# Kernel optimization log

Hardware: AMD Instinct MI355X
Metric: run time of the kernel (lower is better)

The kernel has to match this reference:

```python
import jax, jax.numpy as jnp
import numpy as np


def setup_inputs() -> dict:
    key = jax.random.key(0)
    k1, k2, k3 = jax.random.split(key, 3)
    B, S, H, D, W = 2, 2048, 16, 128, 4  # W = world_size (ring steps); k,v carry W*S total KV
    q = jax.random.normal(k1, (B, S, H, D), dtype=jnp.float32)
    k = jax.random.normal(k2, (B, W * S, H, D), dtype=jnp.float32)
    v = jax.random.normal(k3, (B, W * S, H, D), dtype=jnp.float32)
    return {"q": q, "k": k, "v": v}


def _ring_attention(q, k, v):
    # q: [B,S,H,D]; k,v: [B,W*S,H,D] -- W ring steps over KV chunks of length S
    B, S, H, D = q.shape
    W = k.shape[1] // S
    scale = D ** -0.5
    kc = k.reshape(B, W, S, H, D).transpose(1, 0, 2, 3, 4)  # [W,B,S,H,D]
    vc = v.reshape(B, W, S, H, D).transpose(1, 0, 2, 3, 4)
    o0 = jnp.zeros((B, H, S, D), q.dtype)
    l0 = jnp.zeros((B, H, S, 1), q.dtype)
    m0 = jnp.full((B, H, S, 1), -jnp.inf, q.dtype)

    def step(carry, kv):
        o, l, m = carry
        kb, vb = kv  # [B,S,H,D]
        scores = jnp.einsum('bqhd,bkhd->bhqk', q, kb) * scale  # [B,H,S,S]
        m_blk = jnp.max(scores, axis=-1, keepdims=True)
        p = jnp.exp(scores - m_blk)
        l_blk = jnp.sum(p, axis=-1, keepdims=True)
        m_new = jnp.maximum(m, m_blk)
        alpha = jnp.exp(m - m_blk * 0 - m_new) if False else jnp.exp(m - m_new)
        beta = jnp.exp(m_blk - m_new)
        l_new = alpha * l + beta * l_blk
        o_blk = jnp.einsum('bhqk,bkhd->bhqd', p, vb)
        o_new = (alpha * o * l + beta * o_blk) / l_new  # online-softmax rescale (same as torch code)
        return (o_new, l_new, m_new), None

    (o, l, m), _ = jax.lax.scan(step, (o0, l0, m0), (kc, vc))
    return o.transpose(0, 2, 1, 3)  # back to [B,S,H,D]


def reference(q, k, v):
    return _ring_attention(q, k, v)
```

## Files before the change

### kernel.cpp

```cpp
#include <hip/hip_runtime.h>

namespace {
constexpr int Bc  = 2;
constexpr int Sq  = 2048;
constexpr int Hn  = 16;
constexpr int Dd  = 128;
constexpr int Skv = 8192;
constexpr int TK  = 64;
constexpr int NT  = Skv / TK;
constexpr int QT  = 256;
constexpr int PP  = 72;
constexpr int PV  = 132;
constexpr int TILE_ELEMS = TK * Dd;
constexpr int QTF = 128;
constexpr int KPF = 136;
constexpr float C_EXP = (float)(0.08838834764831845 * 1.4426950408889634);
}

typedef __attribute__((ext_vector_type(8))) short short8;
typedef __attribute__((ext_vector_type(8))) unsigned short us8;
typedef __attribute__((ext_vector_type(4))) float f32x4;
typedef __attribute__((ext_vector_type(4))) unsigned short us4;

__device__ __forceinline__ unsigned short f2bf(float f) {
  unsigned int u = __builtin_bit_cast(unsigned int, f);
  u += 0x7fffu + ((u >> 16) & 1u);
  return (unsigned short)(u >> 16);
}

__device__ __forceinline__ void gload16(const unsigned short* g, unsigned short* l) {
  __builtin_amdgcn_global_load_lds(
      (__attribute__((address_space(1))) void*)(g),
      (__attribute__((address_space(3))) void*)(l), 16, 0, 0);
}

__global__ __launch_bounds__(256) void convert_kernel(
    const float* __restrict__ kg, const float* __restrict__ vg,
    unsigned short* __restrict__ kws, unsigned short* __restrict__ vws) {
  __shared__ unsigned short lds_v[TK * PV];

  const int t = threadIdx.x;
  const int bid = blockIdx.x;
  const int bh = bid >> 7;
  const int tile = bid & 127;
  const int b = bh >> 4, h = bh & (Hn - 1);
  const size_t HD = (size_t)Hn * Dd;

  const float* kin = kg + ((size_t)b * Skv + (size_t)tile * TK) * HD + (size_t)h * Dd;
  const float* vin = vg + ((size_t)b * Skv + (size_t)tile * TK) * HD + (size_t)h * Dd;
  unsigned short* kout = kws + (size_t)bid * TILE_ELEMS;
  unsigned short* vout = vws + (size_t)bid * TILE_ELEMS;

  {
    const int key = t >> 2;
    const int c   = t & 3;
    const float* vrow = vin + (size_t)key * HD + c * 32;
    unsigned short* lrow = &lds_v[key * PV + c * 32];
#pragma unroll
    for (int j = 0; j < 8; ++j) {
      float4 a = *(const float4*)(vrow + 4 * j);
      us4 w;
      w[0] = f2bf(a.x); w[1] = f2bf(a.y); w[2] = f2bf(a.z); w[3] = f2bf(a.w);
      *(us4*)&lrow[4 * j] = w;
    }
  }

  {
    const int key = t >> 2;
    const float* krow = kin + (size_t)key * HD;
    unsigned short* orow = kout + key * Dd;
#pragma unroll
    for (int i = 0; i < 4; ++i) {
      const int dblk = (t & 3) * 4 + i;
      const int dsrc = dblk ^ (key & 7);
      float4 a = *(const float4*)(krow + dsrc * 8);
      float4 c4 = *(const float4*)(krow + dsrc * 8 + 4);
      us8 w;
      w[0] = f2bf(a.x);  w[1] = f2bf(a.y);  w[2] = f2bf(a.z);  w[3] = f2bf(a.w);
      w[4] = f2bf(c4.x); w[5] = f2bf(c4.y); w[6] = f2bf(c4.z); w[7] = f2bf(c4.w);
      *(us8*)&orow[dblk * 8] = w;
    }
  }

  __syncthreads();

  {
    const int d = t >> 1;
    const int half = t & 1;
    const int f = (d >> 1) & 7;
#pragma unroll
    for (int jj = 0; jj < 4; ++jj) {
      const int kp = half * 4 + jj;
      const int sb = kp ^ f;
      us8 w;
#pragma unroll
      for (int r = 0; r < 8; ++r) w[r] = lds_v[(sb * 8 + r) * PV + d];
      *(us8*)&vout[d * TK + kp * 8] = w;
    }
  }
}

__global__ __launch_bounds__(512, 2) void ring_attn_bf16(
    const float* __restrict__ qg, const unsigned short* __restrict__ kws,
    const unsigned short* __restrict__ vws, float* __restrict__ og) {
  __shared__ unsigned short lds_k[2][TK * Dd];
  __shared__ unsigned short lds_vt[2][Dd * TK];
  __shared__ unsigned short lds_p[8 * 32 * PP];

  const int t    = threadIdx.x;
  const int wave = t >> 6;
  const int lane = t & 63;
  const int l15  = lane & 15;
  const int quad = lane >> 4;
  const int bid  = blockIdx.x;
  const int bh = ((bid & 7) << 2) | (bid >> 6);
  const int qt = (bid >> 3) & 7;
  const int h  = bh & (Hn - 1);
  const int b  = bh >> 4;
  const size_t HD = (size_t)Hn * Dd;

  const unsigned short* kbh = kws + (size_t)bh * (NT * (size_t)TILE_ELEMS);
  const unsigned short* vbh = vws + (size_t)bh * (NT * (size_t)TILE_ELEMS);
  const int c0 = wave * 1024 + lane * 8;

#pragma unroll
  for (int j = 0; j < 2; ++j) {
    gload16(kbh + c0 + j * 512, &lds_k[0][wave * 1024 + j * 512]);
    gload16(vbh + c0 + j * 512, &lds_vt[0][wave * 1024 + j * 512]);
  }

  short8 qfrag[2][4];
  {
    const float* qbase = qg + ((size_t)b * Sq) * HD + (size_t)h * Dd;
#pragma unroll
    for (int mt = 0; mt < 2; ++mt) {
      const int qrow = qt * QT + wave * 32 + mt * 16 + l15;
      const float* qp = qbase + (size_t)qrow * HD;
#pragma unroll
      for (int kk = 0; kk < 4; ++kk) {
        const float* p8 = qp + kk * 32 + quad * 8;
        float4 a = *(const float4*)p8;
        float4 c = *(const float4*)(p8 + 4);
        short8 f;
        f[0] = (short)f2bf(a.x); f[1] = (short)f2bf(a.y);
        f[2] = (short)f2bf(a.z); f[3] = (short)f2bf(a.w);
        f[4] = (short)f2bf(c.x); f[5] = (short)f2bf(c.y);
        f[6] = (short)f2bf(c.z); f[7] = (short)f2bf(c.w);
        qfrag[mt][kk] = f;
      }
    }
  }

  f32x4 acco[2][8];
#pragma unroll
  for (int mt = 0; mt < 2; ++mt)
#pragma unroll
    for (int n = 0; n < 8; ++n)
      acco[mt][n] = (f32x4){0.f, 0.f, 0.f, 0.f};

  float l_part[2] = {0.f, 0.f};

  int koff[4], voff[2];
#pragma unroll
  for (int kk = 0; kk < 4; ++kk) koff[kk] = ((kk * 4 + quad) ^ (l15 & 7)) * 8;
#pragma unroll
  for (int kk = 0; kk < 2; ++kk) voff[kk] = ((kk * 4 + quad) ^ ((l15 >> 1) & 7)) * 8;

  asm volatile("s_waitcnt vmcnt(0)" ::: "memory");
  __syncthreads();

  int buf = 0;
  for (int it = 0; it < NT; ++it) {
    if (it + 1 < NT) {
      const unsigned short* kt = kbh + (size_t)(it + 1) * TILE_ELEMS;
      const unsigned short* vt = vbh + (size_t)(it + 1) * TILE_ELEMS;
      unsigned short* kd = &lds_k[buf ^ 1][wave * 1024];
      unsigned short* vd = &lds_vt[buf ^ 1][wave * 1024];
#pragma unroll
      for (int j = 0; j < 2; ++j) {
        gload16(kt + c0 + j * 512, kd + j * 512);
        gload16(vt + c0 + j * 512, vd + j * 512);
      }
    }

    const unsigned short* kb = &lds_k[buf][0];
    f32x4 accs[2][4];
#pragma unroll
    for (int mt = 0; mt < 2; ++mt)
#pragma unroll
      for (int n = 0; n < 4; ++n)
        accs[mt][n] = (f32x4){0.f, 0.f, 0.f, 0.f};

    __builtin_amdgcn_s_setprio(1);
#pragma unroll
    for (int n = 0; n < 4; ++n) {
      short8 bfr[4];
#pragma unroll
      for (int kk = 0; kk < 4; ++kk)
        bfr[kk] = *(const short8*)&kb[(n * 16 + l15) * Dd + koff[kk]];
#pragma unroll
      for (int mt = 0; mt < 2; ++mt)
#pragma unroll
        for (int kk = 0; kk < 4; ++kk)
          accs[mt][n] = __builtin_amdgcn_mfma_f32_16x16x32_bf16(
              bfr[kk], qfrag[mt][kk], accs[mt][n], 0, 0, 0);
    }
    __builtin_amdgcn_s_setprio(0);

#pragma unroll
    for (int mt = 0; mt < 2; ++mt) {
      float lacc = 0.f;
#pragma unroll
      for (int n = 0; n < 4; ++n) {
        float s0 = __builtin_amdgcn_exp2f(accs[mt][n][0] * C_EXP);
        float s1 = __builtin_amdgcn_exp2f(accs[mt][n][1] * C_EXP);
        float s2 = __builtin_amdgcn_exp2f(accs[mt][n][2] * C_EXP);
        float s3 = __builtin_amdgcn_exp2f(accs[mt][n][3] * C_EXP);
        lacc += (s0 + s1) + (s2 + s3);
        us4 w;
        w[0] = f2bf(s0); w[1] = f2bf(s1); w[2] = f2bf(s2); w[3] = f2bf(s3);
        *(us4*)&lds_p[wave * (32 * PP) + (mt * 16 + l15) * PP + n * 16 + quad * 4] = w;
      }
      l_part[mt] += lacc;
    }

    asm volatile("s_waitcnt lgkmcnt(0)" ::: "memory");

    const unsigned short* vb = &lds_vt[buf][0];
    __builtin_amdgcn_s_setprio(1);
#pragma unroll
    for (int kk = 0; kk < 2; ++kk) {
      short8 afr[2];
#pragma unroll
      for (int mt = 0; mt < 2; ++mt)
        afr[mt] = *(const short8*)&lds_p[wave * (32 * PP) + (mt * 16 + l15) * PP +
                                         kk * 32 + quad * 8];
#pragma unroll
      for (int n = 0; n < 8; ++n) {
        short8 bfr = *(const short8*)&vb[(n * 16 + l15) * TK + voff[kk]];
        acco[0][n] = __builtin_amdgcn_mfma_f32_16x16x32_bf16(afr[0], bfr, acco[0][n], 0, 0, 0);
        acco[1][n] = __builtin_amdgcn_mfma_f32_16x16x32_bf16(afr[1], bfr, acco[1][n], 0, 0, 0);
      }
    }
    __builtin_amdgcn_s_setprio(0);

    asm volatile("s_waitcnt vmcnt(0)" ::: "memory");
    __syncthreads();
    buf ^= 1;
  }

#pragma unroll
  for (int mt = 0; mt < 2; ++mt) {
    float l = l_part[mt];
    l += __shfl_xor(l, 16);
    l += __shfl_xor(l, 32);
    l_part[mt] = l;
  }

  float* ob = og + ((size_t)b * Sq) * HD + (size_t)h * Dd;
#pragma unroll
  for (int mt = 0; mt < 2; ++mt) {
#pragma unroll
    for (int i = 0; i < 4; ++i) {
      const int qrow = qt * QT + wave * 32 + mt * 16 + quad * 4 + i;
      const float inv = 1.0f / __shfl(l_part[mt], quad * 4 + i);
      float* op = ob + (size_t)qrow * HD;
#pragma unroll
      for (int n = 0; n < 8; ++n)
        op[n * 16 + l15] = acco[mt][n][i] * inv;
    }
  }
}

__global__ __launch_bounds__(256) void ring_attn_fallback(
    const float* __restrict__ qg, const float* __restrict__ kg,
    const float* __restrict__ vg, float* __restrict__ og) {
  __shared__ unsigned short lds_k[TK * KPF];
  __shared__ unsigned short lds_vt[Dd * 64];
  __shared__ unsigned short lds_p[4 * 32 * PP];

  const int t    = threadIdx.x;
  const int wave = t >> 6;
  const int lane = t & 63;
  const int l15  = lane & 15;
  const int quad = lane >> 4;
  const int bid  = blockIdx.x;
  const int bh = ((bid & 7) << 2) | (bid >> 7);
  const int qt = (bid >> 3) & 15;
  const int h  = bh & (Hn - 1);
  const int b  = bh >> 4;
  const size_t HD = (size_t)Hn * Dd;

  short8 qfrag[2][4];
  {
    const float* qbase = qg + ((size_t)b * Sq) * HD + (size_t)h * Dd;
    for (int mt = 0; mt < 2; ++mt) {
      const int qrow = qt * QTF + wave * 32 + mt * 16 + l15;
      const float* qp = qbase + (size_t)qrow * HD;
#pragma unroll
      for (int kk = 0; kk < 4; ++kk) {
        const float* p8 = qp + kk * 32 + quad * 8;
        float4 a = *(const float4*)p8;
        float4 c = *(const float4*)(p8 + 4);
        short8 f;
        f[0] = (short)f2bf(a.x); f[1] = (short)f2bf(a.y);
        f[2] = (short)f2bf(a.z); f[3] = (short)f2bf(a.w);
        f[4] = (short)f2bf(c.x); f[5] = (short)f2bf(c.y);
        f[6] = (short)f2bf(c.z); f[7] = (short)f2bf(c.w);
        qfrag[mt][kk] = f;
      }
    }
  }

  f32x4 acco[2][8];
#pragma unroll
  for (int mt = 0; mt < 2; ++mt)
#pragma unroll
    for (int n = 0; n < 8; ++n)
      acco[mt][n] = (f32x4){0.f, 0.f, 0.f, 0.f};

  float l_part[2][4];
#pragma unroll
  for (int mt = 0; mt < 2; ++mt)
#pragma unroll
    for (int i = 0; i < 4; ++i) l_part[mt][i] = 0.f;

  const float* kb_g = kg + ((size_t)b * Skv) * HD + (size_t)h * Dd;
  const float* vb_g = vg + ((size_t)b * Skv) * HD + (size_t)h * Dd;
  const int th = t >> 5;
  const int tl = t & 31;
  const int dq = tl << 2;

  for (int it = 0; it < Skv / TK; ++it) {
    const int kv0 = it * TK;
    __syncthreads();

#pragma unroll
    for (int r = 0; r < 8; ++r) {
      const int key = th + r * 8;
      float4 k4 = *(const float4*)(kb_g + (size_t)(kv0 + key) * HD + dq);
      us4 kw;
      kw[0] = f2bf(k4.x); kw[1] = f2bf(k4.y);
      kw[2] = f2bf(k4.z); kw[3] = f2bf(k4.w);
      *(us4*)&lds_k[key * KPF + dq] = kw;
    }

    {
      const int vK0 = th << 3;
      us4 vreg[8];
#pragma unroll
      for (int r = 0; r < 8; ++r) {
        float4 v4 = *(const float4*)(vb_g + (size_t)(kv0 + vK0 + r) * HD + dq);
        vreg[r][0] = f2bf(v4.x); vreg[r][1] = f2bf(v4.y);
        vreg[r][2] = f2bf(v4.z); vreg[r][3] = f2bf(v4.w);
      }
      const int kbp = (th ^ (tl & 7)) << 3;
#pragma unroll
      for (int i = 0; i < 4; ++i) {
        const int d = dq + i;
        us8 w;
#pragma unroll
        for (int r = 0; r < 8; ++r) w[r] = vreg[r][i];
        *(us8*)&lds_vt[d * 64 + kbp] = w;
      }
    }
    __syncthreads();

    f32x4 accs[2][4];
#pragma unroll
    for (int mt = 0; mt < 2; ++mt)
#pragma unroll
      for (int n = 0; n < 4; ++n)
        accs[mt][n] = (f32x4){0.f, 0.f, 0.f, 0.f};

#pragma unroll
    for (int n = 0; n < 4; ++n) {
      short8 bfr[4];
#pragma unroll
      for (int kk = 0; kk < 4; ++kk)
        bfr[kk] = *(const short8*)&lds_k[(n * 16 + l15) * KPF + kk * 32 + quad * 8];
#pragma unroll
      for (int mt = 0; mt < 2; ++mt)
#pragma unroll
        for (int kk = 0; kk < 4; ++kk)
          accs[mt][n] = __builtin_amdgcn_mfma_f32_16x16x32_bf16(
              qfrag[mt][kk], bfr[kk], accs[mt][n], 0, 0, 0);
    }

#pragma unroll
    for (int mt = 0; mt < 2; ++mt) {
#pragma unroll
      for (int i = 0; i < 4; ++i) {
        float s0 = __builtin_amdgcn_exp2f(accs[mt][0][i] * C_EXP);
        float s1 = __builtin_amdgcn_exp2f(accs[mt][1][i] * C_EXP);
        float s2 = __builtin_amdgcn_exp2f(accs[mt][2][i] * C_EXP);
        float s3 = __builtin_amdgcn_exp2f(accs[mt][3][i] * C_EXP);
        accs[mt][0][i] = s0; accs[mt][1][i] = s1;
        accs[mt][2][i] = s2; accs[mt][3][i] = s3;
        l_part[mt][i] += (s0 + s1) + (s2 + s3);
      }
#pragma unroll
      for (int n = 0; n < 4; ++n)
#pragma unroll
        for (int i = 0; i < 4; ++i)
          lds_p[wave * (32 * PP) + (mt * 16 + quad * 4 + i) * PP + n * 16 + l15] =
              f2bf(accs[mt][n][i]);
    }

    asm volatile("s_waitcnt lgkmcnt(0)" ::: "memory");

#pragma unroll
    for (int kk = 0; kk < 2; ++kk) {
      short8 afr[2];
#pragma unroll
      for (int mt = 0; mt < 2; ++mt)
        afr[mt] = *(const short8*)&lds_p[wave * (32 * PP) + (mt * 16 + l15) * PP +
                                         kk * 32 + quad * 8];
#pragma unroll
      for (int n = 0; n < 8; ++n) {
        const int dcol = n * 16 + l15;
        const int kbr = ((quad + 4 * kk) ^ ((dcol >> 2) & 7)) << 3;
        short8 bfr = *(const short8*)&lds_vt[dcol * 64 + kbr];
        acco[0][n] = __builtin_amdgcn_mfma_f32_16x16x32_bf16(afr[0], bfr, acco[0][n], 0, 0, 0);
        acco[1][n] = __builtin_amdgcn_mfma_f32_16x16x32_bf16(afr[1], bfr, acco[1][n], 0, 0, 0);
      }
    }
  }

#pragma unroll
  for (int mt = 0; mt < 2; ++mt)
#pragma unroll
    for (int i = 0; i < 4; ++i) {
      float l = l_part[mt][i];
#pragma unroll
      for (int off = 1; off < 16; off <<= 1) l += __shfl_xor(l, off);
      l_part[mt][i] = l;
    }

  float* ob = og + ((size_t)b * Sq) * HD + (size_t)h * Dd;
#pragma unroll
  for (int mt = 0; mt < 2; ++mt) {
#pragma unroll
    for (int i = 0; i < 4; ++i) {
      const int qrow = qt * QTF + wave * 32 + mt * 16 + quad * 4 + i;
      const float inv = 1.0f / l_part[mt][i];
      float* op = ob + (size_t)qrow * HD;
#pragma unroll
      for (int n = 0; n < 8; ++n)
        op[n * 16 + l15] = acco[mt][n][i] * inv;
    }
  }
}

extern "C" void kernel_launch(void* const* d_in, const int* in_sizes, int n_in,
                              void* d_out, int out_size, void* d_ws, size_t ws_size,
                              hipStream_t stream) {
  const float* q = (const float*)d_in[0];
  const float* k = (const float*)d_in[1];
  const float* v = (const float*)d_in[2];
  float* out = (float*)d_out;

  constexpr size_t KWS_ELEMS = (size_t)Bc * Hn * NT * TILE_ELEMS;
  constexpr size_t WS_NEED = 2 * KWS_ELEMS * sizeof(unsigned short);

  if (d_ws != nullptr && ws_size >= WS_NEED) {
    unsigned short* kws = (unsigned short*)d_ws;
    unsigned short* vws = kws + KWS_ELEMS;
    convert_kernel<<<dim3(Bc * Hn * NT), dim3(256), 0, stream>>>(k, v, kws, vws);
    ring_attn_bf16<<<dim3(Bc * Hn * (Sq / QT)), dim3(512), 0, stream>>>(q, kws, vws, out);
  } else {
    ring_attn_fallback<<<dim3(Bc * Hn * (Sq / QTF)), dim3(256), 0, stream>>>(q, k, v, out);
  }
}
```

Before: 660.7 us.

## Keep softmax probabilities in registers via lane shuffles; halve attention block size

The attention kernel no longer writes the bf16 probability tile to LDS and reads it back. It packs pairs of probabilities with v_cvt_pk_bf16_f32 and rearranges them into MFMA A-operand layout using __shfl across lanes. Blocks shrink from 512 to 256 threads (128 query rows each), which doubles the grid, and each wave loads twice as much of every K/V tile. The convert kernel now stages both K and V in padded LDS and writes fully contiguous 16-byte chunks. The aim is to remove the LDS round-trip and its wait for P, at the cost of extra shuffle instructions and per-wave load work.

```diff
diff --git a/kernel.cpp b/kernel.cpp
--- a/kernel.cpp
+++ b/kernel.cpp
@@ -8,12 +8,12 @@
 constexpr int Skv = 8192;
 constexpr int TK  = 64;
 constexpr int NT  = Skv / TK;
-constexpr int QT  = 256;
-constexpr int PP  = 72;
-constexpr int PV  = 132;
+constexpr int QT  = 128;
+constexpr int PC  = 132;
 constexpr int TILE_ELEMS = TK * Dd;
 constexpr int QTF = 128;
 constexpr int KPF = 136;
+constexpr int PP  = 72;
 constexpr float C_EXP = (float)(0.08838834764831845 * 1.4426950408889634);
 }
 
@@ -21,6 +21,7 @@
 typedef __attribute__((ext_vector_type(8))) unsigned short us8;
 typedef __attribute__((ext_vector_type(4))) float f32x4;
 typedef __attribute__((ext_vector_type(4))) unsigned short us4;
+typedef __attribute__((ext_vector_type(4))) unsigned int u32x4;
 
 __device__ __forceinline__ unsigned short f2bf(float f) {
   unsigned int u = __builtin_bit_cast(unsigned int, f);
@@ -28,6 +29,12 @@
   return (unsigned short)(u >> 16);
 }
 
+__device__ __forceinline__ unsigned int cvtpk(float lo, float hi) {
+  unsigned int r;
+  asm("v_cvt_pk_bf16_f32 %0, %1, %2" : "=v"(r) : "v"(lo), "v"(hi));
+  return r;
+}
+
 __device__ __forceinline__ void gload16(const unsigned short* g, unsigned short* l) {
   __builtin_amdgcn_global_load_lds(
       (__attribute__((address_space(1))) void*)(g),
@@ -37,7 +44,8 @@
 __global__ __launch_bounds__(256) void convert_kernel(
     const float* __restrict__ kg, const float* __restrict__ vg,
     unsigned short* __restrict__ kws, unsigned short* __restrict__ vws) {
-  __shared__ unsigned short lds_v[TK * PV];
+  __shared__ unsigned short lds_kc[TK * PC];
+  __shared__ unsigned short lds_vc[TK * PC];
 
   const int t = threadIdx.x;
   const int bid = blockIdx.x;
@@ -54,230 +62,56 @@
   {
     const int key = t >> 2;
     const int c   = t & 3;
+    const float* krow = kin + (size_t)key * HD + c * 32;
     const float* vrow = vin + (size_t)key * HD + c * 32;
-    unsigned short* lrow = &lds_v[key * PV + c * 32];
+    unsigned short* lk = &lds_kc[key * PC + c * 32];
+    unsigned short* lv = &lds_vc[key * PC + c * 32];
 #pragma unroll
     for (int j = 0; j < 8; ++j) {
-      float4 a = *(const float4*)(vrow + 4 * j);
+      float4 a = *(const float4*)(krow + 4 * j);
       us4 w;
       w[0] = f2bf(a.x); w[1] = f2bf(a.y); w[2] = f2bf(a.z); w[3] = f2bf(a.w);
-      *(us4*)&lrow[4 * j] = w;
-    }
-  }
-
-  {
-    const int key = t >> 2;
-    const float* krow = kin + (size_t)key * HD;
-    unsigned short* orow = kout + key * Dd;
-#pragma unroll
-    for (int i = 0; i < 4; ++i) {
-      const int dblk = (t & 3) * 4 + i;
-      const int dsrc = dblk ^ (key & 7);
-      float4 a = *(const float4*)(krow + dsrc * 8);
-      float4 c4 = *(const float4*)(krow + dsrc * 8 + 4);
-      us8 w;
-      w[0] = f2bf(a.x);  w[1] = f2bf(a.y);  w[2] = f2bf(a.z);  w[3] = f2bf(a.w);
-      w[4] = f2bf(c4.x); w[5] = f2bf(c4.y); w[6] = f2bf(c4.z); w[7] = f2bf(c4.w);
-      *(us8*)&orow[dblk * 8] = w;
+      *(us4*)&lk[4 * j] = w;
+      float4 v = *(const float4*)(vrow + 4 * j);
+      us4 u;
+      u[0] = f2bf(v.x); u[1] = f2bf(v.y); u[2] = f2bf(v.z); u[3] = f2bf(v.w);
+      *(us4*)&lv[4 * j] = u;
     }
   }
 
   __syncthreads();
 
-  {
-    const int d = t >> 1;
-    const int half = t & 1;
-    const int f = (d >> 1) & 7;
-#pragma unroll
-    for (int jj = 0; jj < 4; ++jj) {
-      const int kp = half * 4 + jj;
-      const int sb = kp ^ f;
-      us8 w;
-#pragma unroll
-      for (int r = 0; r < 8; ++r) w[r] = lds_v[(sb * 8 + r) * PV + d];
-      *(us8*)&vout[d * TK + kp * 8] = w;
-    }
-  }
-}
-
-__global__ __launch_bounds__(512, 2) void ring_attn_bf16(
+#pragma unroll
+  for (int it = 0; it < 4; ++it) {
+    const int c = it * 256 + t;
+    const int key = c >> 4;
+    const int dp = c & 15;
+    const int dsrc = dp ^ (key & 7);
+    us4 r0 = *(const us4*)&lds_kc[key * PC + dsrc * 8];
+    us4 r1 = *(const us4*)&lds_kc[key * PC + dsrc * 8 + 4];
+    us8 w;
+    w[0] = r0[0]; w[1] = r0[1]; w[2] = r0[2]; w[3] = r0[3];
+    w[4] = r1[0]; w[5] = r1[1]; w[6] = r1[2]; w[7] = r1[3];
+    *(us8*)&kout[c * 8] = w;
+  }
+#pragma unroll
+  for (int it = 0; it < 4; ++it) {
+    const int c = it * 256 + t;
+    const int d = c >> 3;
+    const int kp = c & 7;
+    const int sb = kp ^ ((d >> 1) & 7);
+    us8 w;
+#pragma unroll
+    for (int r = 0; r < 8; ++r) w[r] = lds_vc[(sb * 8 + r) * PC + d];
+    *(us8*)&vout[c * 8] = w;
+  }
+}
+
+__global__ __launch_bounds__(256, 2) void ring_attn_bf16(
     const float* __restrict__ qg, const unsigned short* __restrict__ kws,
     const unsigned short* __restrict__ vws, float* __restrict__ og) {
   __shared__ unsigned short lds_k[2][TK * Dd];
   __shared__ unsigned short lds_vt[2][Dd * TK];
-  __shared__ unsigned short lds_p[8 * 32 * PP];
-
-  const int t    = threadIdx.x;
-  const int wave = t >> 6;
-  const int lane = t & 63;
-  const int l15  = lane & 15;
-  const int quad = lane >> 4;
-  const int bid  = blockIdx.x;
-  const int bh = ((bid & 7) << 2) | (bid >> 6);
-  const int qt = (bid >> 3) & 7;
-  const int h  = bh & (Hn - 1);
-  const int b  = bh >> 4;
-  const size_t HD = (size_t)Hn * Dd;
-
-  const unsigned short* kbh = kws + (size_t)bh * (NT * (size_t)TILE_ELEMS);
-  const unsigned short* vbh = vws + (size_t)bh * (NT * (size_t)TILE_ELEMS);
-  const int c0 = wave * 1024 + lane * 8;
-
-#pragma unroll
-  for (int j = 0; j < 2; ++j) {
-    gload16(kbh + c0 + j * 512, &lds_k[0][wave * 1024 + j * 512]);
-    gload16(vbh + c0 + j * 512, &lds_vt[0][wave * 1024 + j * 512]);
-  }
-
-  short8 qfrag[2][4];
-  {
-    const float* qbase = qg + ((size_t)b * Sq) * HD + (size_t)h * Dd;
-#pragma unroll
-    for (int mt = 0; mt < 2; ++mt) {
-      const int qrow = qt * QT + wave * 32 + mt * 16 + l15;
-      const float* qp = qbase + (size_t)qrow * HD;
-#pragma unroll
-      for (int kk = 0; kk < 4; ++kk) {
-        const float* p8 = qp + kk * 32 + quad * 8;
-        float4 a = *(const float4*)p8;
-        float4 c = *(const float4*)(p8 + 4);
-        short8 f;
-        f[0] = (short)f2bf(a.x); f[1] = (short)f2bf(a.y);
-        f[2] = (short)f2bf(a.z); f[3] = (short)f2bf(a.w);
-        f[4] = (short)f2bf(c.x); f[5] = (short)f2bf(c.y);
-        f[6] = (short)f2bf(c.z); f[7] = (short)f2bf(c.w);
-        qfrag[mt][kk] = f;
-      }
-    }
-  }
-
-  f32x4 acco[2][8];
-#pragma unroll
-  for (int mt = 0; mt < 2; ++mt)
-#pragma unroll
-    for (int n = 0; n < 8; ++n)
-      acco[mt][n] = (f32x4){0.f, 0.f, 0.f, 0.f};
-
-  float l_part[2] = {0.f, 0.f};
-
-  int koff[4], voff[2];
-#pragma unroll
-  for (int kk = 0; kk < 4; ++kk) koff[kk] = ((kk * 4 + quad) ^ (l15 & 7)) * 8;
-#pragma unroll
-  for (int kk = 0; kk < 2; ++kk) voff[kk] = ((kk * 4 + quad) ^ ((l15 >> 1) & 7)) * 8;
-
-  asm volatile("s_waitcnt vmcnt(0)" ::: "memory");
-  __syncthreads();
-
-  int buf = 0;
-  for (int it = 0; it < NT; ++it) {
-    if (it + 1 < NT) {
-      const unsigned short* kt = kbh + (size_t)(it + 1) * TILE_ELEMS;
-      const unsigned short* vt = vbh + (size_t)(it + 1) * TILE_ELEMS;
-      unsigned short* kd = &lds_k[buf ^ 1][wave * 1024];
-      unsigned short* vd = &lds_vt[buf ^ 1][wave * 1024];
-#pragma unroll
-      for (int j = 0; j < 2; ++j) {
-        gload16(kt + c0 + j * 512, kd + j * 512);
-        gload16(vt + c0 + j * 512, vd + j * 512);
-      }
-    }
-
-    const unsigned short* kb = &lds_k[buf][0];
-    f32x4 accs[2][4];
-#pragma unroll
-    for (int mt = 0; mt < 2; ++mt)
-#pragma unroll
-      for (int n = 0; n < 4; ++n)
-        accs[mt][n] = (f32x4){0.f, 0.f, 0.f, 0.f};
-
-    __builtin_amdgcn_s_setprio(1);
-#pragma unroll
-    for (int n = 0; n < 4; ++n) {
-      short8 bfr[4];
-#pragma unroll
-      for (int kk = 0; kk < 4; ++kk)
-        bfr[kk] = *(const short8*)&kb[(n * 16 + l15) * Dd + koff[kk]];
-#pragma unroll
-      for (int mt = 0; mt < 2; ++mt)
-#pragma unroll
-        for (int kk = 0; kk < 4; ++kk)
-          accs[mt][n] = __builtin_amdgcn_mfma_f32_16x16x32_bf16(
-              bfr[kk], qfrag[mt][kk], accs[mt][n], 0, 0, 0);
-    }
-    __builtin_amdgcn_s_setprio(0);
-
-#pragma unroll
-    for (int mt = 0; mt < 2; ++mt) {
-      float lacc = 0.f;
-#pragma unroll
-      for (int n = 0; n < 4; ++n) {
-        float s0 = __builtin_amdgcn_exp2f(accs[mt][n][0] * C_EXP);
-        float s1 = __builtin_amdgcn_exp2f(accs[mt][n][1] * C_EXP);
-        float s2 = __builtin_amdgcn_exp2f(accs[mt][n][2] * C_EXP);
-        float s3 = __builtin_amdgcn_exp2f(accs[mt][n][3] * C_EXP);
-        lacc += (s0 + s1) + (s2 + s3);
-        us4 w;
-        w[0] = f2bf(s0); w[1] = f2bf(s1); w[2] = f2bf(s2); w[3] = f2bf(s3);
-        *(us4*)&lds_p[wave * (32 * PP) + (mt * 16 + l15) * PP + n * 16 + quad * 4] = w;
-      }
-      l_part[mt] += lacc;
-    }
-
-    asm volatile("s_waitcnt lgkmcnt(0)" ::: "memory");
-
-    const unsigned short* vb = &lds_vt[buf][0];
-    __builtin_amdgcn_s_setprio(1);
-#pragma unroll
-    for (int kk = 0; kk < 2; ++kk) {
-      short8 afr[2];
-#pragma unroll
-      for (int mt = 0; mt < 2; ++mt)
-        afr[mt] = *(const short8*)&lds_p[wave * (32 * PP) + (mt * 16 + l15) * PP +
-                                         kk * 32 + quad * 8];
-#pragma unroll
-      for (int n = 0; n < 8; ++n) {
-        short8 bfr = *(const short8*)&vb[(n * 16 + l15) * TK + voff[kk]];
-        acco[0][n] = __builtin_amdgcn_mfma_f32_16x16x32_bf16(afr[0], bfr, acco[0][n], 0, 0, 0);
-        acco[1][n] = __builtin_amdgcn_mfma_f32_16x16x32_bf16(afr[1], bfr, acco[1][n], 0, 0, 0);
-      }
-    }
-    __builtin_amdgcn_s_setprio(0);
-
-    asm volatile("s_waitcnt vmcnt(0)" ::: "memory");
-    __syncthreads();
-    buf ^= 1;
-  }
-
-#pragma unroll
-  for (int mt = 0; mt < 2; ++mt) {
-    float l = l_part[mt];
-    l += __shfl_xor(l, 16);
-    l += __shfl_xor(l, 32);
-    l_part[mt] = l;
-  }
-
-  float* ob = og + ((size_t)b * Sq) * HD + (size_t)h * Dd;
-#pragma unroll
-  for (int mt = 0; mt < 2; ++mt) {
-#pragma unroll
-    for (int i = 0; i < 4; ++i) {
-      const int qrow = qt * QT + wave * 32 + mt * 16 + quad * 4 + i;
-      const float inv = 1.0f / __shfl(l_part[mt], quad * 4 + i);
-      float* op = ob + (size_t)qrow * HD;
-#pragma unroll
-      for (int n = 0; n < 8; ++n)
-        op[n * 16 + l15] = acco[mt][n][i] * inv;
-    }
-  }
-}
-
-__global__ __launch_bounds__(256) void ring_attn_fallback(
-    const float* __restrict__ qg, const float* __restrict__ kg,
-    const float* __restrict__ vg, float* __restrict__ og) {
-  __shared__ unsigned short lds_k[TK * KPF];
-  __shared__ unsigned short lds_vt[Dd * 64];
-  __shared__ unsigned short lds_p[4 * 32 * PP];
 
   const int t    = threadIdx.x;
   const int wave = t >> 6;
@@ -291,11 +125,22 @@
   const int b  = bh >> 4;
   const size_t HD = (size_t)Hn * Dd;
 
+  const unsigned short* kbh = kws + (size_t)bh * (NT * (size_t)TILE_ELEMS);
+  const unsigned short* vbh = vws + (size_t)bh * (NT * (size_t)TILE_ELEMS);
+  const int c0 = wave * 2048 + lane * 8;
+
+#pragma unroll
+  for (int j = 0; j < 4; ++j) {
+    gload16(kbh + c0 + j * 512, &lds_k[0][wave * 2048 + j * 512]);
+    gload16(vbh + c0 + j * 512, &lds_vt[0][wave * 2048 + j * 512]);
+  }
+
   short8 qfrag[2][4];
   {
     const float* qbase = qg + ((size_t)b * Sq) * HD + (size_t)h * Dd;
+#pragma unroll
     for (int mt = 0; mt < 2; ++mt) {
-      const int qrow = qt * QTF + wave * 32 + mt * 16 + l15;
+      const int qrow = qt * QT + wave * 32 + mt * 16 + l15;
       const float* qp = qbase + (size_t)qrow * HD;
 #pragma unroll
       for (int kk = 0; kk < 4; ++kk) {
@@ -319,6 +164,179 @@
     for (int n = 0; n < 8; ++n)
       acco[mt][n] = (f32x4){0.f, 0.f, 0.f, 0.f};
 
+  float l_part[2] = {0.f, 0.f};
+
+  int koff[4], voff[2];
+#pragma unroll
+  for (int kk = 0; kk < 4; ++kk) koff[kk] = ((kk * 4 + quad) ^ (l15 & 7)) * 8;
+#pragma unroll
+  for (int kk = 0; kk < 2; ++kk) voff[kk] = ((kk * 4 + quad) ^ ((l15 >> 1) & 7)) * 8;
+
+  const int sl0 = ((quad & 1) << 5) + l15;
+
+  asm volatile("s_waitcnt vmcnt(0)" ::: "memory");
+  __syncthreads();
+
+  int buf = 0;
+  for (int it = 0; it < NT; ++it) {
+    if (it + 1 < NT) {
+      const unsigned short* kt = kbh + (size_t)(it + 1) * TILE_ELEMS;
+      const unsigned short* vt = vbh + (size_t)(it + 1) * TILE_ELEMS;
+      unsigned short* kd = &lds_k[buf ^ 1][wave * 2048];
+      unsigned short* vd = &lds_vt[buf ^ 1][wave * 2048];
+#pragma unroll
+      for (int j = 0; j < 4; ++j) {
+        gload16(kt + c0 + j * 512, kd + j * 512);
+        gload16(vt + c0 + j * 512, vd + j * 512);
+      }
+    }
+
+    const unsigned short* kb = &lds_k[buf][0];
+    f32x4 accs[2][4];
+#pragma unroll
+    for (int mt = 0; mt < 2; ++mt)
+#pragma unroll
+      for (int n = 0; n < 4; ++n)
+        accs[mt][n] = (f32x4){0.f, 0.f, 0.f, 0.f};
+
+    __builtin_amdgcn_s_setprio(1);
+#pragma unroll
+    for (int n = 0; n < 4; ++n) {
+      short8 bfr[4];
+#pragma unroll
+      for (int kk = 0; kk < 4; ++kk)
+        bfr[kk] = *(const short8*)&kb[(n * 16 + l15) * Dd + koff[kk]];
+#pragma unroll
+      for (int mt = 0; mt < 2; ++mt)
+#pragma unroll
+        for (int kk = 0; kk < 4; ++kk)
+          accs[mt][n] = __builtin_amdgcn_mfma_f32_16x16x32_bf16(
+              bfr[kk], qfrag[mt][kk], accs[mt][n], 0, 0, 0);
+    }
+    __builtin_amdgcn_s_setprio(0);
+
+    short8 afr[2][2];
+#pragma unroll
+    for (int mt = 0; mt < 2; ++mt) {
+      unsigned int pk[4][2];
+      float lacc = 0.f;
+#pragma unroll
+      for (int n = 0; n < 4; ++n) {
+        float s0 = __builtin_amdgcn_exp2f(accs[mt][n][0] * C_EXP);
+        float s1 = __builtin_amdgcn_exp2f(accs[mt][n][1] * C_EXP);
+        float s2 = __builtin_amdgcn_exp2f(accs[mt][n][2] * C_EXP);
+        float s3 = __builtin_amdgcn_exp2f(accs[mt][n][3] * C_EXP);
+        lacc += (s0 + s1) + (s2 + s3);
+        pk[n][0] = cvtpk(s0, s1);
+        pk[n][1] = cvtpk(s2, s3);
+      }
+      l_part[mt] += lacc;
+#pragma unroll
+      for (int kk = 0; kk < 2; ++kk) {
+        unsigned int v[4];
+#pragma unroll
+        for (int hh = 0; hh < 2; ++hh) {
+          const int src = sl0 + (hh << 4);
+#pragma unroll
+          for (int w = 0; w < 2; ++w) {
+            unsigned int a = (unsigned int)__shfl((int)pk[2 * kk][w], src);
+            unsigned int bb = (unsigned int)__shfl((int)pk[2 * kk + 1][w], src);
+            v[hh * 2 + w] = (quad & 2) ? bb : a;
+          }
+        }
+        u32x4 u = {v[0], v[1], v[2], v[3]};
+        afr[mt][kk] = __builtin_bit_cast(short8, u);
+      }
+    }
+
+    const unsigned short* vb = &lds_vt[buf][0];
+    __builtin_amdgcn_s_setprio(1);
+#pragma unroll
+    for (int kk = 0; kk < 2; ++kk) {
+#pragma unroll
+      for (int n = 0; n < 8; ++n) {
+        short8 bfr = *(const short8*)&vb[(n * 16 + l15) * TK + voff[kk]];
+        acco[0][n] = __builtin_amdgcn_mfma_f32_16x16x32_bf16(afr[0][kk], bfr, acco[0][n], 0, 0, 0);
+        acco[1][n] = __builtin_amdgcn_mfma_f32_16x16x32_bf16(afr[1][kk], bfr, acco[1][n], 0, 0, 0);
+      }
+    }
+    __builtin_amdgcn_s_setprio(0);
+
+    asm volatile("s_waitcnt vmcnt(0)" ::: "memory");
+    __syncthreads();
+    buf ^= 1;
+  }
+
+#pragma unroll
+  for (int mt = 0; mt < 2; ++mt) {
+    float l = l_part[mt];
+    l += __shfl_xor(l, 16);
+    l += __shfl_xor(l, 32);
+    l_part[mt] = l;
+  }
+
+  float* ob = og + ((size_t)b * Sq) * HD + (size_t)h * Dd;
+#pragma unroll
+  for (int mt = 0; mt < 2; ++mt) {
+#pragma unroll
+    for (int i = 0; i < 4; ++i) {
+      const int qrow = qt * QT + wave * 32 + mt * 16 + quad * 4 + i;
+      const float inv = 1.0f / __shfl(l_part[mt], quad * 4 + i);
+      float* op = ob + (size_t)qrow * HD;
+#pragma unroll
+      for (int n = 0; n < 8; ++n)
+        op[n * 16 + l15] = acco[mt][n][i] * inv;
+    }
+  }
+}
+
+__global__ __launch_bounds__(256) void ring_attn_fallback(
+    const float* __restrict__ qg, const float* __restrict__ kg,
+    const float* __restrict__ vg, float* __restrict__ og) {
+  __shared__ unsigned short lds_k[TK * KPF];
+  __shared__ unsigned short lds_vt[Dd * 64];
+  __shared__ unsigned short lds_p[4 * 32 * PP];
+
+  const int t    = threadIdx.x;
+  const int wave = t >> 6;
+  const int lane = t & 63;
+  const int l15  = lane & 15;
+  const int quad = lane >> 4;
+  const int bid  = blockIdx.x;
+  const int bh = ((bid & 7) << 2) | (bid >> 7);
+  const int qt = (bid >> 3) & 15;
+  const int h  = bh & (Hn - 1);
+  const int b  = bh >> 4;
+  const size_t HD = (size_t)Hn * Dd;
+
+  short8 qfrag[2][4];
+  {
+    const float* qbase = qg + ((size_t)b * Sq) * HD + (size_t)h * Dd;
+    for (int mt = 0; mt < 2; ++mt) {
+      const int qrow = qt * QTF + wave * 32 + mt * 16 + l15;
+      const float* qp = qbase + (size_t)qrow * HD;
+#pragma unroll
+      for (int kk = 0; kk < 4; ++kk) {
+        const float* p8 = qp + kk * 32 + quad * 8;
+        float4 a = *(const float4*)p8;
+        float4 c = *(const float4*)(p8 + 4);
+        short8 f;
+        f[0] = (short)f2bf(a.x); f[1] = (short)f2bf(a.y);
+        f[2] = (short)f2bf(a.z); f[3] = (short)f2bf(a.w);
+        f[4] = (short)f2bf(c.x); f[5] = (short)f2bf(c.y);
+        f[6] = (short)f2bf(c.z); f[7] = (short)f2bf(c.w);
+        qfrag[mt][kk] = f;
+      }
+    }
+  }
+
+  f32x4 acco[2][8];
+#pragma unroll
+  for (int mt = 0; mt < 2; ++mt)
+#pragma unroll
+    for (int n = 0; n < 8; ++n)
+      acco[mt][n] = (f32x4){0.f, 0.f, 0.f, 0.f};
+
   float l_part[2][4];
 #pragma unroll
   for (int mt = 0; mt < 2; ++mt)
@@ -467,7 +485,7 @@
     unsigned short* kws = (unsigned short*)d_ws;
     unsigned short* vws = kws + KWS_ELEMS;
     convert_kernel<<<dim3(Bc * Hn * NT), dim3(256), 0, stream>>>(k, v, kws, vws);
-    ring_attn_bf16<<<dim3(Bc * Hn * (Sq / QT)), dim3(512), 0, stream>>>(q, kws, vws, out);
+    ring_attn_bf16<<<dim3(Bc * Hn * (Sq / QT)), dim3(256), 0, stream>>>(q, kws, vws, out);
   } else {
     ring_attn_fallback<<<dim3(Bc * Hn * (Sq / QTF)), dim3(256), 0, stream>>>(q, k, v, out);
   }
```

Result: faster. 639.1 us (-3.3%).
